# Kernel tuning notes

Hardware: AMD Instinct MI355X
Metric: run time of the kernel (lower is better)

## Reference

```python
import jax, jax.numpy as jnp
import numpy as np

S, B, E, H, O, WL, PL, T = 128, 64, 1024, 1024, 135, 64, 32, 100


def setup_inputs() -> dict:
    key = jax.random.key(0)
    ks = jax.random.split(key, 12)
    rn = lambda k, shape, s=1.0: jax.random.normal(k, shape, jnp.float32) * s
    return dict(
        encoder_states=rn(ks[0], (S, B, E)),
        encoder_hidden=rn(ks[1], (2, B, E // 2)),
        previous_poses=rn(ks[2], (PL, B, O)),
        words=rn(ks[3], (WL, B, 200)),
        real_poses_len=T,
        W_ed=rn(ks[4], (H, E), 0.02), b_ed=jnp.zeros((H,), jnp.float32),
        W_att=rn(ks[5], (H, E), 0.02), b_att=jnp.zeros((H,), jnp.float32),
        W_watt=rn(ks[6], (H, 200), 0.02), b_watt=jnp.zeros((H,), jnp.float32),
        W_ih=rn(ks[7], (3 * H, O), 0.02), W_hh=rn(ks[8], (3 * H, H), 0.02),
        b_ih=jnp.zeros((3 * H,), jnp.float32), b_hh=jnp.zeros((3 * H,), jnp.float32),
        W_out=rn(ks[9], (O, 3 * H), 0.02), b_out=jnp.zeros((O,), jnp.float32),
    )


def _gru_step(x, h, W_ih, W_hh, b_ih, b_hh):
    # PyTorch GRU cell: gates ordered (r, z, n)
    gi = x @ W_ih.T + b_ih  # [B, 3H]
    gh = h @ W_hh.T + b_hh  # [B, 3H]
    Hd = h.shape[-1]
    ir, iz, inn = gi[:, :Hd], gi[:, Hd:2 * Hd], gi[:, 2 * Hd:]
    hr, hz, hn = gh[:, :Hd], gh[:, Hd:2 * Hd], gh[:, 2 * Hd:]
    r = jax.nn.sigmoid(ir + hr)
    z = jax.nn.sigmoid(iz + hz)
    n = jnp.tanh(inn + r * hn)
    return (1.0 - z) * n + z * h


def _attend(proj, h):
    # proj: [S, B, H] (already enc_to_dec-projected), h: [B, H]
    scores = jnp.einsum('sbh,bh->bs', proj, h)
    w = jax.nn.softmax(scores, axis=1)
    return jnp.einsum('sbh,bs->bh', proj, w)  # [B, H]


def reference(encoder_states, encoder_hidden, previous_poses, words, real_poses_len,
              W_ed, b_ed, W_att, b_att, W_watt, b_watt,
              W_ih, W_hh, b_ih, b_hh, W_out, b_out):
    s, b, e = encoder_states.shape
    # take last bidirectional layer, merge directions -> [B, E]
    eh = encoder_hidden.reshape(-1, 2, b, e // 2)[-1]          # [2, B, E/2]
    h = jnp.transpose(eh, (1, 0, 2)).reshape(b, e) @ W_ed.T + b_ed  # [B, H]

    # warm-up GRU pass over previous poses (only final hidden is used)
    def warm(hc, x):
        return _gru_step(x, hc, W_ih, W_hh, b_ih, b_hh), None
    h, _ = jax.lax.scan(warm, h, previous_poses)

    # attention projections are step-invariant: hoist out of the loop
    enc_proj = encoder_states @ W_att.T + b_att   # [S, B, H]
    word_proj = words @ W_watt.T + b_watt         # [WL, B, H]

    start = previous_poses[-1]                    # [B, O]

    def step(carry, _):
        pose, hc = carry
        hc = _gru_step(pose, hc, W_ih, W_hh, b_ih, b_hh)
        ctx = _attend(enc_proj, hc)
        wctx = _attend(word_proj, hc)
        cat = jnp.concatenate([hc, ctx, wctx], axis=1)  # [B, 3H]; dropout = identity (eval)
        pose = cat @ W_out.T + b_out                    # [B, O]
        return (pose, hc), pose

    _, poses = jax.lax.scan(step, (start, h), None, length=real_poses_len)
    return poses  # [T, B, O]
```

## Files before the change

### kernel.cpp

```cpp
#include <hip/hip_runtime.h>
#include <cstdint>
#include <cstddef>

typedef unsigned short ushort_t;
typedef __attribute__((ext_vector_type(8))) short short8;
typedef __attribute__((ext_vector_type(4))) float floatx4;

#define SS 128
#define BB 64
#define EE 1024
#define HH 1024
#define OO 135
#define WLW 64
#define PLP 32
#define TT 100
#define KP 160
#define NWG 64
#define NTH 1024

#define WHH_PITCH 1032
#define WIH_PITCH 168
#define LDS_WHH   0
#define LDS_WIH   99072
#define LDS_CX    115200
#define LDS_SC    127488
#define LDS_WTS   128256
#define LDS_RED   115200
#define RED_GATE  304
#define RED_BT    1216
#define RED_REG   4864

#define FB_DTYPE 0
#define FB_FLAGS 32

static __device__ __forceinline__ float bf2f(ushort_t u) {
    union { unsigned int i; float f; } v; v.i = ((unsigned int)u) << 16; return v.f;
}
static __device__ __forceinline__ ushort_t f2bf(float f) {
    union { float f; unsigned int i; } v; v.f = f;
    unsigned int x = v.i;
    x += 0x7fffu + ((x >> 16) & 1u);
    return (ushort_t)(x >> 16);
}
static __device__ __forceinline__ float ldf(const void* p, long i, unsigned isbf) {
    if (isbf) return bf2f(((const ushort_t*)p)[i]);
    return ((const float*)p)[i];
}
static __device__ __forceinline__ short8 ldfrag(const ushort_t* p) {
    return *reinterpret_cast<const short8*>(p);
}
static __device__ __forceinline__ short8 ldfrag_l(const short* p) {
    return *reinterpret_cast<const short8*>(p);
}
static __device__ __forceinline__ int cxp(int m) {
    return ((m & 15) << 6) | (m >> 4);
}
static __device__ __forceinline__ unsigned long long sysld_u64(const void* p) {
    return __hip_atomic_load((const unsigned long long*)p, __ATOMIC_RELAXED, __HIP_MEMORY_SCOPE_AGENT);
}
static __device__ __forceinline__ void sysst_u16(ushort_t* p, ushort_t v) {
    __hip_atomic_store(p, v, __ATOMIC_RELAXED, __HIP_MEMORY_SCOPE_AGENT);
}
static __device__ __forceinline__ void sysst_u32(unsigned* p, unsigned v) {
    __hip_atomic_store(p, v, __ATOMIC_RELAXED, __HIP_MEMORY_SCOPE_SYSTEM);
}
static __device__ __forceinline__ unsigned sysld_u32(const unsigned* p) {
    return __hip_atomic_load(p, __ATOMIC_RELAXED, __HIP_MEMORY_SCOPE_SYSTEM);
}
static __device__ __forceinline__ short8 sysld_frag16(const ushort_t* p) {
    union { unsigned long long u[2]; short8 s; } r;
    r.u[0] = sysld_u64(p);
    r.u[1] = sysld_u64(p + 4);
    return r.s;
}
static __device__ __forceinline__ short8 frag_ld(const void* p, unsigned isbf,
                                                 long rowoff, int kbase, int kcap) {
    if (kbase >= kcap) {
        short8 z = {0, 0, 0, 0, 0, 0, 0, 0};
        return z;
    }
    if (isbf) return ldfrag((const ushort_t*)p + rowoff + kbase);
    const float* f = (const float*)p + rowoff + kbase;
    short8 a;
    #pragma unroll
    for (int i = 0; i < 8; ++i) a[i] = (short)f2bf(f[i]);
    return a;
}
static __device__ __forceinline__ floatx4 mfma(short8 a, short8 b, floatx4 c) {
    return __builtin_amdgcn_mfma_f32_16x16x32_bf16(a, b, c, 0, 0, 0);
}
static __device__ __forceinline__ float sigmoidf(float x) {
    x = fminf(fmaxf(x, -30.f), 30.f);
    return 1.f / (1.f + __expf(-x));
}
static __device__ __forceinline__ float tanh_f(float x) {
    x = fminf(fmaxf(x, -15.f), 15.f);
    float e = __expf(2.f * x);
    return (e - 1.f) / (e + 1.f);
}

static __device__ __forceinline__ void gbar(unsigned* flags, unsigned phase) {
    __syncthreads();
    if (threadIdx.x < 64) {
        __builtin_amdgcn_fence(__ATOMIC_RELEASE, "workgroup");
        if (threadIdx.x == 0)
            sysst_u32(&flags[(size_t)blockIdx.x * 32], phase);
        for (;;) {
            unsigned v = sysld_u32(&flags[(size_t)threadIdx.x * 32]);
            if (__all((int)(v >= phase))) break;
            __builtin_amdgcn_s_sleep(1);
        }
        __builtin_amdgcn_fence(__ATOMIC_ACQUIRE, "workgroup");
    }
    __syncthreads();
}

__global__ void k_detect(const unsigned* __restrict__ enc, unsigned* __restrict__ flag)
{
    __shared__ int cnt;
    if (threadIdx.x == 0) cnt = 0;
    __syncthreads();
    unsigned w = enc[threadIdx.x];
    unsigned ef = (w >> 7) & 0xFFu;
    if (ef >= 0x70u && ef <= 0x81u) atomicAdd(&cnt, 1);
    for (int i = threadIdx.x; i < NWG * 32; i += 256)
        sysst_u32(&flag[FB_FLAGS + i], 0u);
    __syncthreads();
    if (threadIdx.x == 0)
        flag[FB_DTYPE] = (cnt >= 200) ? 1u : 0u;
}

__global__ void k_prep(const void* __restrict__ eh, const void* __restrict__ Wih,
                       const void* __restrict__ Wout, const void* __restrict__ pp,
                       const void* __restrict__ Whh,
                       ushort_t* __restrict__ ehcat, ushort_t* __restrict__ wih_p,
                       ushort_t* __restrict__ wout_p, ushort_t* __restrict__ pp_pad,
                       ushort_t* __restrict__ pose_pad, ushort_t* __restrict__ whh_bf,
                       const unsigned* __restrict__ flag)
{
    unsigned isbf = flag[FB_DTYPE];
    long idx = (long)blockIdx.x * 256 + threadIdx.x;
    const long n1 = BB * EE;
    const long n2 = (long)3 * HH * KP;
    const long n3f = (long)144 * 3 * HH;
    const long n4 = (long)PLP * BB * KP;
    const long n5 = (long)BB * KP;
    const long n6 = (long)3 * HH * HH;
    if (idx < n1) {
        int b = (int)(idx >> 10), r = (int)(idx & 1023);
        int c = r >> 9, jj = r & 511;
        ehcat[idx] = f2bf(ldf(eh, (long)(c * BB + b) * 512 + jj, isbf));
        return;
    }
    idx -= n1;
    if (idx < n2) {
        long row = idx / KP, k = idx % KP;
        wih_p[idx] = (k < OO) ? f2bf(ldf(Wih, row * OO + k, isbf)) : (ushort_t)0; return;
    }
    idx -= n2;
    if (idx < n3f) {
        long row = idx / (3 * HH), k = idx % (3 * HH);
        wout_p[idx] = (row < OO) ? f2bf(ldf(Wout, row * (3 * HH) + k, isbf)) : (ushort_t)0; return;
    }
    idx -= n3f;
    if (idx < n4) {
        long t = idx / (BB * KP); long rem = idx % (BB * KP);
        long b = rem / KP, k = rem % KP;
        pp_pad[idx] = (k < OO) ? f2bf(ldf(pp, (t * BB + b) * OO + k, isbf)) : (ushort_t)0; return;
    }
    idx -= n4;
    if (idx < n5) { pose_pad[idx] = 0; return; }
    idx -= n5;
    if (idx < n6) { whh_bf[idx] = f2bf(ldf(Whh, idx, isbf)); return; }
}

__global__ void __launch_bounds__(256) k_gemm(
    const void* __restrict__ A, int a_bf16, int lda, int kcapA,
    const void* __restrict__ B, int b_bf16, int ldb, int kcapB,
    const void* __restrict__ biasRaw,
    float* __restrict__ outF, ushort_t* __restrict__ outB16,
    ushort_t* __restrict__ outHi, ushort_t* __restrict__ outLo,
    int ldo, int M, int N, int K, const unsigned* __restrict__ flag)
{
    unsigned isbf = flag[FB_DTYPE];
    unsigned a_isbf = a_bf16 ? 1u : isbf;
    unsigned b_isbf = b_bf16 ? 1u : isbf;
    int lane = threadIdx.x & 63;
    int wid = (blockIdx.x << 2) + (threadIdx.x >> 6);
    int ng = N >> 6;
    int mt = wid / ng, g = wid % ng;
    if (mt * 16 >= M) return;
    int col = lane & 15, quad = lane >> 4;
    long arow = (long)(mt * 16 + col) * lda;
    long brow0 = (long)((g << 6) + col) * ldb;
    long brow1 = brow0 + (long)16 * ldb;
    long brow2 = brow0 + (long)32 * ldb;
    long brow3 = brow0 + (long)48 * ldb;
    int kb = quad * 8;
    floatx4 ac0 = {0.f, 0.f, 0.f, 0.f}, ac1 = ac0, ac2 = ac0, ac3 = ac0;
    for (int k = 0; k < K; k += 32) {
        short8 av = frag_ld(A, a_isbf, arow, kb + k, kcapA);
        ac0 = mfma(av, frag_ld(B, b_isbf, brow0, kb + k, kcapB), ac0);
        ac1 = mfma(av, frag_ld(B, b_isbf, brow1, kb + k, kcapB), ac1);
        ac2 = mfma(av, frag_ld(B, b_isbf, brow2, kb + k, kcapB), ac2);
        ac3 = mfma(av, frag_ld(B, b_isbf, brow3, kb + k, kcapB), ac3);
    }
    int m0 = mt * 16 + quad * 4;
    #pragma unroll
    for (int tIdx = 0; tIdx < 4; ++tIdx) {
        floatx4 ac = (tIdx == 0) ? ac0 : (tIdx == 1) ? ac1 : (tIdx == 2) ? ac2 : ac3;
        int n = (g << 6) + tIdx * 16 + col;
        float bv = biasRaw ? ldf(biasRaw, n, isbf) : 0.f;
        #pragma unroll
        for (int r = 0; r < 4; ++r) {
            float v = ac[r] + bv;
            size_t o = (size_t)(m0 + r) * ldo + n;
            if (outF) outF[o] = v;
            if (outB16) outB16[o] = f2bf(v);
            if (outHi) {
                ushort_t hi = f2bf(v);
                outHi[o] = hi;
                outLo[o] = f2bf(v - bf2f(hi));
            }
        }
    }
}

__global__ void __launch_bounds__(1024, 4) k_persist(
    const ushort_t* encP,
    const ushort_t* wordP,
    const ushort_t* __restrict__ whh_bf, const ushort_t* __restrict__ wih_p,
    const void* __restrict__ b_ih, const void* __restrict__ b_hh,
    const ushort_t* __restrict__ wout_p,
    const void* __restrict__ b_out,
    const ushort_t* __restrict__ pp_pad, ushort_t* __restrict__ pose_pad,
    float* hFa, float* hFb, ushort_t* hhia, ushort_t* hhib,
    ushort_t* hloa, ushort_t* hlob,
    void* __restrict__ out, unsigned* flagbar)
{
    extern __shared__ char smem[];
    short* whh_lds = (short*)(smem + LDS_WHH);
    short* wih_lds = (short*)(smem + LDS_WIH);
    float* cx  = (float*)(smem + LDS_CX);
    float* sc  = (float*)(smem + LDS_SC);
    float* wts = (float*)(smem + LDS_WTS);
    float* red = (float*)(smem + LDS_RED);

    const int tid = threadIdx.x;
    const int lane = tid & 63, wv = tid >> 6;
    const int wg = blockIdx.x;
    const int col = lane & 15, quad = lane >> 4;
    const int bt = wv & 3;
    const int ks = wv >> 2;
    unsigned isbf = flagbar[FB_DTYPE];
    unsigned* flags = flagbar + FB_FLAGS;
    unsigned bphase = 0;

    float* hFs = hFa; float* hFd = hFb;
    ushort_t* hhis = hhia; ushort_t* hhid = hhib;
    ushort_t* hlos = hloa; ushort_t* hlod = hlob;

    for (int s = tid; s < 48 * 128; s += NTH) {
        int r = s >> 7;
        int ko = (s & 127) << 3;
        int g = r >> 4, rr = r & 15;
        *(short8*)(whh_lds + r * WHH_PITCH + ko) =
            ldfrag(whh_bf + (size_t)g * HH * HH + (size_t)(wg * 16 + rr) * HH + ko);
    }
    for (int s = tid; s < 48 * 20; s += NTH) {
        int r = s / 20;
        int ko = (s % 20) << 3;
        int g = r >> 4, rr = r & 15;
        *(short8*)(wih_lds + r * WIH_PITCH + ko) =
            ldfrag(wih_p + (size_t)g * HH * KP + (size_t)(wg * 16 + rr) * KP + ko);
    }
    __syncthreads();

    const int j = wg * 16 + col;
    const float bir = ldf(b_ih, j, isbf)          + ldf(b_hh, j, isbf);
    const float biz = ldf(b_ih, HH + j, isbf)     + ldf(b_hh, HH + j, isbf);
    const float bin = ldf(b_ih, 2 * HH + j, isbf);
    const float bhn = ldf(b_hh, 2 * HH + j, isbf);

    for (int t = 0; t < PLP + TT; ++t) {
        const bool dec = (t >= PLP);
        const bool warm_src = (t <= PLP);
        const ushort_t* poseA = (t < PLP)  ? (pp_pad + (size_t)t * BB * KP)
                              : (t == PLP) ? (pp_pad + (size_t)(PLP - 1) * BB * KP)
                                           : pose_pad;
        {
            const ushort_t* ah = hhis + (size_t)(bt * 16 + col) * HH + quad * 8;
            const ushort_t* al = hlos + (size_t)(bt * 16 + col) * HH + quad * 8;
            const short* w0 = whh_lds + (size_t)(0  + col) * WHH_PITCH + quad * 8;
            const short* w1 = whh_lds + (size_t)(16 + col) * WHH_PITCH + quad * 8;
            const short* w2 = whh_lds + (size_t)(32 + col) * WHH_PITCH + quad * 8;
            floatx4 aR = {0.f, 0.f, 0.f, 0.f}, aZ = aR, aNi = aR, aNh = aR;
            const int k0 = ks * 256, k1 = k0 + 256;
            #pragma unroll 4
            for (int k = k0; k < k1; k += 32) {
                short8 f0 = ldfrag_l(w0 + k), f1 = ldfrag_l(w1 + k), f2 = ldfrag_l(w2 + k);
                short8 xh = sysld_frag16(ah + k), xl = sysld_frag16(al + k);
                aR = mfma(xh, f0, aR);   aR = mfma(xl, f0, aR);
                aZ = mfma(xh, f1, aZ);   aZ = mfma(xl, f1, aZ);
                aNh = mfma(xh, f2, aNh); aNh = mfma(xl, f2, aNh);
            }
            const ushort_t* ap = poseA + (size_t)(bt * 16 + col) * KP + quad * 8;
            const short* c0 = wih_lds + (size_t)(0  + col) * WIH_PITCH + quad * 8;
            const short* c1 = wih_lds + (size_t)(16 + col) * WIH_PITCH + quad * 8;
            const short* c2 = wih_lds + (size_t)(32 + col) * WIH_PITCH + quad * 8;
            for (int k5 = ks; k5 < 5; k5 += 4) {
                int k = k5 * 32;
                short8 xp = warm_src ? ldfrag(ap + k) : sysld_frag16(ap + k);
                aR = mfma(xp, ldfrag_l(c0 + k), aR);
                aZ = mfma(xp, ldfrag_l(c1 + k), aZ);
                aNi = mfma(xp, ldfrag_l(c2 + k), aNi);
            }
            if (ks == 1 || ks == 3) {
                float* dst = red + (ks >> 1) * RED_REG + bt * RED_BT;
                #pragma unroll
                for (int r = 0; r < 4; ++r) {
                    int idx = (quad * 4 + r) * 19 + col;
                    dst[idx] = aR[r];                  dst[RED_GATE + idx] = aZ[r];
                    dst[2 * RED_GATE + idx] = aNh[r];  dst[3 * RED_GATE + idx] = aNi[r];
                }
            }
            __syncthreads();
            if (ks == 0 || ks == 2) {
                const float* sp = red + (ks >> 1) * RED_REG + bt * RED_BT;
                #pragma unroll
                for (int r = 0; r < 4; ++r) {
                    int idx = (quad * 4 + r) * 19 + col;
                    aR[r] += sp[idx];                  aZ[r] += sp[RED_GATE + idx];
                    aNh[r] += sp[2 * RED_GATE + idx];  aNi[r] += sp[3 * RED_GATE + idx];
                }
            }
            __syncthreads();
            if (ks == 2) {
                float* dst = red + bt * RED_BT;
                #pragma unroll
                for (int r = 0; r < 4; ++r) {
                    int idx = (quad * 4 + r) * 19 + col;
                    dst[idx] = aR[r];                  dst[RED_GATE + idx] = aZ[r];
                    dst[2 * RED_GATE + idx] = aNh[r];  dst[3 * RED_GATE + idx] = aNi[r];
                }
            }
            __syncthreads();
            if (ks == 0) {
                const float* sp = red + bt * RED_BT;
                #pragma unroll
                for (int r = 0; r < 4; ++r) {
                    int idx = (quad * 4 + r) * 19 + col;
                    aR[r] += sp[idx];                  aZ[r] += sp[RED_GATE + idx];
                    aNh[r] += sp[2 * RED_GATE + idx];  aNi[r] += sp[3 * RED_GATE + idx];
                }
                #pragma unroll
                for (int r = 0; r < 4; ++r) {
                    int b = bt * 16 + quad * 4 + r;
                    float hold = hFs[(size_t)b * HH + j];
                    float rg = sigmoidf(aR[r] + bir);
                    float zg = sigmoidf(aZ[r] + biz);
                    float ng = tanh_f(aNi[r] + bin + rg * (aNh[r] + bhn));
                    float hn = (1.f - zg) * ng + zg * hold;
                    hFd[(size_t)b * HH + j] = hn;
                    ushort_t hi = f2bf(hn);
                    sysst_u16(&hhid[(size_t)b * HH + j], hi);
                    sysst_u16(&hlod[(size_t)b * HH + j], f2bf(hn - bf2f(hi)));
                }
            }
        }
        { float* tf = hFs; hFs = hFd; hFd = tf; }
        { ushort_t* tp = hhis; hhis = hhid; hhid = tp;
          tp = hlos; hlos = hlod; hlod = tp; }
        ++bphase;
        gbar(flags, bphase);
        if (!dec) continue;

        {
            const int b = wg;
            if (tid < 256) {
                union { unsigned long long u; ushort_t e[4]; } h4, l4;
                h4.u = sysld_u64(hhis + (size_t)b * HH + tid * 4);
                l4.u = sysld_u64(hlos + (size_t)b * HH + tid * 4);
                #pragma unroll
                for (int i = 0; i < 4; ++i)
                    cx[cxp(tid * 4 + i)] = bf2f(h4.e[i]) + bf2f(l4.e[i]);
            }
            __syncthreads();
            float hreg[16];
            #pragma unroll
            for (int i = 0; i < 16; ++i) hreg[i] = cx[(i << 6) | lane];
            const ushort_t* rows = encP;
            #pragma unroll 2
            for (int idx = wv; idx < 192; idx += 16) {
                const ushort_t* rp = rows + ((size_t)(idx * BB + b) << 10);
                short8 v0 = ldfrag(rp + lane * 16);
                short8 v1 = ldfrag(rp + lane * 16 + 8);
                float s = 0.f;
                #pragma unroll
                for (int i = 0; i < 8; ++i) s += bf2f((ushort_t)v0[i]) * hreg[i];
                #pragma unroll
                for (int i = 0; i < 8; ++i) s += bf2f((ushort_t)v1[i]) * hreg[8 + i];
                #pragma unroll
                for (int m = 1; m < 64; m <<= 1) s += __shfl_xor(s, m);
                if (lane == 0) sc[idx] = s;
            }
            __syncthreads();
            if (wv == 0) {
                float a = sc[lane], c = sc[lane + 64];
                float mx = fmaxf(a, c);
                #pragma unroll
                for (int m = 1; m < 64; m <<= 1) mx = fmaxf(mx, __shfl_xor(mx, m));
                float e0 = __expf(a - mx), e1 = __expf(c - mx);
                float sm = e0 + e1;
                #pragma unroll
                for (int m = 1; m < 64; m <<= 1) sm += __shfl_xor(sm, m);
                float inv = 1.f / sm;
                wts[lane] = e0 * inv; wts[lane + 64] = e1 * inv;
            } else if (wv == 1) {
                float a = sc[128 + lane];
                float mx = a;
                #pragma unroll
                for (int m = 1; m < 64; m <<= 1) mx = fmaxf(mx, __shfl_xor(mx, m));
                float e0 = __expf(a - mx);
                float sm = e0;
                #pragma unroll
                for (int m = 1; m < 64; m <<= 1) sm += __shfl_xor(sm, m);
                wts[128 + lane] = e0 / sm;
            }
            __syncthreads();
            if (tid < 256) {
                float a0 = 0.f, a1 = 0.f, a2 = 0.f, a3 = 0.f;
                const ushort_t* basep = encP + ((size_t)b << 10) + tid * 4;
                #pragma unroll 8
                for (int s = 0; s < SS; ++s) {
                    float w = wts[s];
                    union { unsigned long long u; ushort_t e[4]; } v;
                    v.u = *(const unsigned long long*)(basep + ((size_t)(s * BB) << 10));
                    a0 += w * bf2f(v.e[0]); a1 += w * bf2f(v.e[1]);
                    a2 += w * bf2f(v.e[2]); a3 += w * bf2f(v.e[3]);
                }
                cx[1024 + cxp(tid * 4 + 0)] = a0; cx[1024 + cxp(tid * 4 + 1)] = a1;
                cx[1024 + cxp(tid * 4 + 2)] = a2; cx[1024 + cxp(tid * 4 + 3)] = a3;
            } else if (tid < 512) {
                int tt = tid - 256;
                float a0 = 0.f, a1 = 0.f, a2 = 0.f, a3 = 0.f;
                const ushort_t* basep = wordP + ((size_t)b << 10) + tt * 4;
                #pragma unroll 8
                for (int s = 0; s < WLW; ++s) {
                    float w = wts[128 + s];
                    union { unsigned long long u; ushort_t e[4]; } v;
                    v.u = *(const unsigned long long*)(basep + ((size_t)(s * BB) << 10));
                    a0 += w * bf2f(v.e[0]); a1 += w * bf2f(v.e[1]);
                    a2 += w * bf2f(v.e[2]); a3 += w * bf2f(v.e[3]);
                }
                cx[2048 + cxp(tt * 4 + 0)] = a0; cx[2048 + cxp(tt * 4 + 1)] = a1;
                cx[2048 + cxp(tt * 4 + 2)] = a2; cx[2048 + cxp(tt * 4 + 3)] = a3;
            }
            __syncthreads();
            float cr[48];
            #pragma unroll
            for (int c3 = 0; c3 < 3; ++c3)
                #pragma unroll
                for (int i = 0; i < 16; ++i)
                    cr[c3 * 16 + i] = cx[c3 * 1024 + (i << 6) + lane];
            int td = t - PLP;
            for (int oo = 0; oo < 9; ++oo) {
                int o = wv * 9 + oo;
                const ushort_t* wr = wout_p + (size_t)o * (3 * HH) + lane * 16;
                float s = 0.f;
                #pragma unroll
                for (int c3 = 0; c3 < 3; ++c3) {
                    short8 w8a = ldfrag(wr + c3 * 1024);
                    short8 w8b = ldfrag(wr + c3 * 1024 + 8);
                    #pragma unroll
                    for (int i = 0; i < 8; ++i) s += bf2f((ushort_t)w8a[i]) * cr[c3 * 16 + i];
                    #pragma unroll
                    for (int i = 0; i < 8; ++i) s += bf2f((ushort_t)w8b[i]) * cr[c3 * 16 + 8 + i];
                }
                #pragma unroll
                for (int m = 1; m < 64; m <<= 1) s += __shfl_xor(s, m);
                if (lane == 0) {
                    float v = s + ((o < OO) ? ldf(b_out, o, isbf) : 0.f);
                    if (o < OO) {
                        size_t oi = ((size_t)td * BB + b) * OO + o;
                        if (isbf) ((ushort_t*)out)[oi] = f2bf(v);
                        else      ((float*)out)[oi] = v;
                    }
                    sysst_u16(&pose_pad[(size_t)b * KP + o], (o < OO) ? f2bf(v) : (ushort_t)0);
                }
            }
        }
        ++bphase;
        gbar(flags, bphase);
    }
}

extern "C" void kernel_launch(void* const* d_in, const int* in_sizes, int n_in,
                              void* d_out, int out_size, void* d_ws, size_t ws_size,
                              hipStream_t stream)
{
    (void)in_sizes; (void)n_in; (void)out_size; (void)ws_size;
    const void* enc_states = d_in[0];
    const void* enc_hidden = d_in[1];
    const void* prev_poses = d_in[2];
    const void* words      = d_in[3];
    const void* W_ed  = d_in[5];
    const void* b_ed  = d_in[6];
    const void* W_att = d_in[7];
    const void* b_att = d_in[8];
    const void* W_watt = d_in[9];
    const void* b_watt = d_in[10];
    const void* W_ih  = d_in[11];
    const void* W_hh  = d_in[12];
    const void* b_ih  = d_in[13];
    const void* b_hh  = d_in[14];
    const void* W_out = d_in[15];
    const void* b_out = d_in[16];

    char* base = (char*)d_ws;
    size_t off = 0;
    auto alloc = [&](size_t bytes) -> char* {
        char* p = base + off;
        off = (off + bytes + 255) & ~(size_t)255;
        return p;
    };
    unsigned* flagbar  = (unsigned*)alloc(128 + (size_t)NWG * 128);
    ushort_t* ehcat    = (ushort_t*)alloc((size_t)BB * EE * 2);
    ushort_t* wih_p    = (ushort_t*)alloc((size_t)3 * HH * KP * 2);
    ushort_t* wout_p   = (ushort_t*)alloc((size_t)144 * 3 * HH * 2);
    ushort_t* pp_pad   = (ushort_t*)alloc((size_t)PLP * BB * KP * 2);
    ushort_t* pose_pad = (ushort_t*)alloc((size_t)BB * KP * 2);
    ushort_t* whh_bf   = (ushort_t*)alloc((size_t)3 * HH * HH * 2);
    float*    hF0      = (float*)alloc((size_t)BB * HH * 4);
    float*    hF1      = (float*)alloc((size_t)BB * HH * 4);
    ushort_t* hhi0     = (ushort_t*)alloc((size_t)BB * HH * 2);
    ushort_t* hhi1     = (ushort_t*)alloc((size_t)BB * HH * 2);
    ushort_t* hlo0     = (ushort_t*)alloc((size_t)BB * HH * 2);
    ushort_t* hlo1     = (ushort_t*)alloc((size_t)BB * HH * 2);
    ushort_t* encP     = (ushort_t*)alloc((size_t)SS * BB * HH * 2);
    ushort_t* wordP    = (ushort_t*)alloc((size_t)WLW * BB * HH * 2);

    k_detect<<<1, 256, 0, stream>>>((const unsigned*)enc_states, flagbar);

    k_prep<<<17512, 256, 0, stream>>>(enc_hidden, W_ih, W_out, prev_poses, W_hh,
                                      ehcat, wih_p, wout_p, pp_pad, pose_pad, whh_bf,
                                      flagbar);

    k_gemm<<<16, 256, 0, stream>>>(ehcat, 1, EE, EE, W_ed, 0, EE, EE, b_ed,
                                   hF0, nullptr, hhi0, hlo0, HH, BB, HH, EE, flagbar);
    k_gemm<<<2048, 256, 0, stream>>>(enc_states, 0, EE, EE, W_att, 0, EE, EE, b_att,
                                     nullptr, encP, nullptr, nullptr, HH, SS * BB, HH, EE, flagbar);
    k_gemm<<<1024, 256, 0, stream>>>(words, 0, 200, 200, W_watt, 0, 200, 200, b_watt,
                                     nullptr, wordP, nullptr, nullptr, HH, WLW * BB, HH, 224, flagbar);

    (void)hipFuncSetAttribute((const void*)k_persist,
                              hipFuncAttributeMaxDynamicSharedMemorySize, 154112);
    k_persist<<<NWG, NTH, 154112, stream>>>(encP, wordP, whh_bf, wih_p,
                                            b_ih, b_hh, wout_p, b_out, pp_pad, pose_pad,
                                            hF0, hF1, hhi0, hhi1, hlo0, hlo1,
                                            d_out, flagbar);
}
```

Measured before the change: 6.118 ms.

## Use MFMA with hi/lo bf16 split for attention scores and output projection

```diff
diff --git a/kernel.cpp b/kernel.cpp
--- a/kernel.cpp
+++ b/kernel.cpp
@@ -22,9 +22,13 @@
 #define WIH_PITCH 168
 #define LDS_WHH   0
 #define LDS_WIH   99072
-#define LDS_CX    115200
-#define LDS_SC    127488
-#define LDS_WTS   128256
+#define LDS_SC    115200
+#define LDS_WTS   115968
+#define LDS_HBH   116736
+#define LDS_HBL   118784
+#define LDS_CXH   120832
+#define LDS_CXL   124928
+#define LDS_PP    129024
 #define LDS_RED   115200
 #define RED_GATE  304
 #define RED_BT    1216
@@ -51,9 +55,6 @@
 }
 static __device__ __forceinline__ short8 ldfrag_l(const short* p) {
     return *reinterpret_cast<const short8*>(p);
-}
-static __device__ __forceinline__ int cxp(int m) {
-    return ((m & 15) << 6) | (m >> 4);
 }
 static __device__ __forceinline__ unsigned long long sysld_u64(const void* p) {
     return __hip_atomic_load((const unsigned long long*)p, __ATOMIC_RELAXED, __HIP_MEMORY_SCOPE_AGENT);
@@ -241,9 +242,13 @@
     extern __shared__ char smem[];
     short* whh_lds = (short*)(smem + LDS_WHH);
     short* wih_lds = (short*)(smem + LDS_WIH);
-    float* cx  = (float*)(smem + LDS_CX);
     float* sc  = (float*)(smem + LDS_SC);
     float* wts = (float*)(smem + LDS_WTS);
+    ushort_t* hb_hi = (ushort_t*)(smem + LDS_HBH);
+    ushort_t* hb_lo = (ushort_t*)(smem + LDS_HBL);
+    ushort_t* cx_hi = (ushort_t*)(smem + LDS_CXH);
+    ushort_t* cx_lo = (ushort_t*)(smem + LDS_CXL);
+    float* pose_part = (float*)(smem + LDS_PP);
     float* red = (float*)(smem + LDS_RED);
 
     const int tid = threadIdx.x;
@@ -378,31 +383,29 @@
         {
             const int b = wg;
             if (tid < 256) {
-                union { unsigned long long u; ushort_t e[4]; } h4, l4;
-                h4.u = sysld_u64(hhis + (size_t)b * HH + tid * 4);
-                l4.u = sysld_u64(hlos + (size_t)b * HH + tid * 4);
-                #pragma unroll
-                for (int i = 0; i < 4; ++i)
-                    cx[cxp(tid * 4 + i)] = bf2f(h4.e[i]) + bf2f(l4.e[i]);
-            }
-            __syncthreads();
-            float hreg[16];
-            #pragma unroll
-            for (int i = 0; i < 16; ++i) hreg[i] = cx[(i << 6) | lane];
+                int k0b = tid * 4;
+                unsigned long long h4 = sysld_u64(hhis + (size_t)b * HH + k0b);
+                unsigned long long l4 = sysld_u64(hlos + (size_t)b * HH + k0b);
+                *(unsigned long long*)(hb_hi + k0b) = h4;
+                *(unsigned long long*)(hb_lo + k0b) = l4;
+            }
+            __syncthreads();
             const ushort_t* rows = encP;
-            #pragma unroll 2
-            for (int idx = wv; idx < 192; idx += 16) {
-                const ushort_t* rp = rows + ((size_t)(idx * BB + b) << 10);
-                short8 v0 = ldfrag(rp + lane * 16);
-                short8 v1 = ldfrag(rp + lane * 16 + 8);
-                float s = 0.f;
-                #pragma unroll
-                for (int i = 0; i < 8; ++i) s += bf2f((ushort_t)v0[i]) * hreg[i];
-                #pragma unroll
-                for (int i = 0; i < 8; ++i) s += bf2f((ushort_t)v1[i]) * hreg[8 + i];
-                #pragma unroll
-                for (int m = 1; m < 64; m <<= 1) s += __shfl_xor(s, m);
-                if (lane == 0) sc[idx] = s;
+            if (wv < 12) {
+                const ushort_t* ap0 = rows + (((size_t)(wv * 16 + col) * BB + b) << 10) + quad * 8;
+                floatx4 acc = {0.f, 0.f, 0.f, 0.f};
+                #pragma unroll 4
+                for (int ks2 = 0; ks2 < 32; ++ks2) {
+                    short8 av = ldfrag(ap0 + ks2 * 32);
+                    short8 bh = *(const short8*)(hb_hi + ks2 * 32 + quad * 8);
+                    short8 bl = *(const short8*)(hb_lo + ks2 * 32 + quad * 8);
+                    acc = mfma(av, bh, acc);
+                    acc = mfma(av, bl, acc);
+                }
+                if (col == 0) {
+                    #pragma unroll
+                    for (int r = 0; r < 4; ++r) sc[wv * 16 + quad * 4 + r] = acc[r];
+                }
             }
             __syncthreads();
             if (wv == 0) {
@@ -439,8 +442,15 @@
                     a0 += w * bf2f(v.e[0]); a1 += w * bf2f(v.e[1]);
                     a2 += w * bf2f(v.e[2]); a3 += w * bf2f(v.e[3]);
                 }
-                cx[1024 + cxp(tid * 4 + 0)] = a0; cx[1024 + cxp(tid * 4 + 1)] = a1;
-                cx[1024 + cxp(tid * 4 + 2)] = a2; cx[1024 + cxp(tid * 4 + 3)] = a3;
+                union { unsigned long long u; ushort_t e[4]; } hi4, lo4;
+                float vv[4] = {a0, a1, a2, a3};
+                #pragma unroll
+                for (int i = 0; i < 4; ++i) {
+                    hi4.e[i] = f2bf(vv[i]);
+                    lo4.e[i] = f2bf(vv[i] - bf2f(hi4.e[i]));
+                }
+                *(unsigned long long*)(cx_hi + tid * 4) = hi4.u;
+                *(unsigned long long*)(cx_lo + tid * 4) = lo4.u;
             } else if (tid < 512) {
                 int tt = tid - 256;
                 float a0 = 0.f, a1 = 0.f, a2 = 0.f, a3 = 0.f;
@@ -453,41 +463,55 @@
                     a0 += w * bf2f(v.e[0]); a1 += w * bf2f(v.e[1]);
                     a2 += w * bf2f(v.e[2]); a3 += w * bf2f(v.e[3]);
                 }
-                cx[2048 + cxp(tt * 4 + 0)] = a0; cx[2048 + cxp(tt * 4 + 1)] = a1;
-                cx[2048 + cxp(tt * 4 + 2)] = a2; cx[2048 + cxp(tt * 4 + 3)] = a3;
-            }
-            __syncthreads();
-            float cr[48];
-            #pragma unroll
-            for (int c3 = 0; c3 < 3; ++c3)
-                #pragma unroll
-                for (int i = 0; i < 16; ++i)
-                    cr[c3 * 16 + i] = cx[c3 * 1024 + (i << 6) + lane];
+                union { unsigned long long u; ushort_t e[4]; } hi4, lo4;
+                float vv[4] = {a0, a1, a2, a3};
+                #pragma unroll
+                for (int i = 0; i < 4; ++i) {
+                    hi4.e[i] = f2bf(vv[i]);
+                    lo4.e[i] = f2bf(vv[i] - bf2f(hi4.e[i]));
+                }
+                *(unsigned long long*)(cx_hi + 1024 + tt * 4) = hi4.u;
+                *(unsigned long long*)(cx_lo + 1024 + tt * 4) = lo4.u;
+            }
+            __syncthreads();
+            #pragma unroll 2
+            for (int pass = 0; pass < 2; ++pass) {
+                if (pass == 1 && wv >= 2) break;
+                int J = (pass == 0) ? wv : 16 + wv;
+                int tile = J >> 1, kh = J & 1;
+                const ushort_t* wr = wout_p + (size_t)(tile * 16 + col) * 3072
+                                   + kh * 1536 + quad * 8;
+                floatx4 acc = {0.f, 0.f, 0.f, 0.f};
+                #pragma unroll 4
+                for (int ks2 = 0; ks2 < 48; ++ks2) {
+                    int kk = kh * 1536 + ks2 * 32;
+                    short8 av = ldfrag(wr + ks2 * 32);
+                    const ushort_t* bh;
+                    const ushort_t* bl;
+                    if (kk < 1024) { bh = hb_hi + kk + quad * 8; bl = hb_lo + kk + quad * 8; }
+                    else           { bh = cx_hi + (kk - 1024) + quad * 8;
+                                     bl = cx_lo + (kk - 1024) + quad * 8; }
+                    acc = mfma(av, *(const short8*)bh, acc);
+                    acc = mfma(av, *(const short8*)bl, acc);
+                }
+                if (col == 0) {
+                    #pragma unroll
+                    for (int r = 0; r < 4; ++r)
+                        pose_part[J * 16 + quad * 4 + r] = acc[r];
+                }
+            }
+            __syncthreads();
             int td = t - PLP;
-            for (int oo = 0; oo < 9; ++oo) {
-                int o = wv * 9 + oo;
-                const ushort_t* wr = wout_p + (size_t)o * (3 * HH) + lane * 16;
-                float s = 0.f;
-                #pragma unroll
-                for (int c3 = 0; c3 < 3; ++c3) {
-                    short8 w8a = ldfrag(wr + c3 * 1024);
-                    short8 w8b = ldfrag(wr + c3 * 1024 + 8);
-                    #pragma unroll
-                    for (int i = 0; i < 8; ++i) s += bf2f((ushort_t)w8a[i]) * cr[c3 * 16 + i];
-                    #pragma unroll
-                    for (int i = 0; i < 8; ++i) s += bf2f((ushort_t)w8b[i]) * cr[c3 * 16 + 8 + i];
-                }
-                #pragma unroll
-                for (int m = 1; m < 64; m <<= 1) s += __shfl_xor(s, m);
-                if (lane == 0) {
-                    float v = s + ((o < OO) ? ldf(b_out, o, isbf) : 0.f);
-                    if (o < OO) {
-                        size_t oi = ((size_t)td * BB + b) * OO + o;
-                        if (isbf) ((ushort_t*)out)[oi] = f2bf(v);
-                        else      ((float*)out)[oi] = v;
-                    }
-                    sysst_u16(&pose_pad[(size_t)b * KP + o], (o < OO) ? f2bf(v) : (ushort_t)0);
-                }
+            if (tid < 144) {
+                int o = tid, T = o >> 4, r = o & 15;
+                float v = pose_part[(T * 2) * 16 + r] + pose_part[(T * 2 + 1) * 16 + r]
+                        + ((o < OO) ? ldf(b_out, o, isbf) : 0.f);
+                if (o < OO) {
+                    size_t oi = ((size_t)td * BB + b) * OO + o;
+                    if (isbf) ((ushort_t*)out)[oi] = f2bf(v);
+                    else      ((float*)out)[oi] = v;
+                }
+                sysst_u16(&pose_pad[(size_t)b * KP + o], (o < OO) ? f2bf(v) : (ushort_t)0);
             }
         }
         ++bphase;
```

New measurement: 7.917 ms. 1.29x slower.

## Repartition GRU step: stream weights from global, stage h tile in LDS

Applied to the files above, without the earlier changes.

```diff
diff --git a/kernel.cpp b/kernel.cpp
--- a/kernel.cpp
+++ b/kernel.cpp
@@ -18,17 +18,16 @@
 #define NWG 64
 #define NTH 1024
 
-#define WHH_PITCH 1032
-#define WIH_PITCH 168
-#define LDS_WHH   0
-#define LDS_WIH   99072
-#define LDS_CX    115200
-#define LDS_SC    127488
-#define LDS_WTS   128256
-#define LDS_RED   115200
+#define LDS_HSH   0
+#define LDS_HSL   33024
+#define LDS_CX    66048
+#define LDS_SC    78336
+#define LDS_WTS   79104
+#define LDS_RED   66048
 #define RED_GATE  304
-#define RED_BT    1216
+#define RED_JS    1216
 #define RED_REG   4864
+#define SMEM_SZ   104960
 
 #define FB_DTYPE 0
 #define FB_FLAGS 32
@@ -239,8 +238,8 @@
     void* __restrict__ out, unsigned* flagbar)
 {
     extern __shared__ char smem[];
-    short* whh_lds = (short*)(smem + LDS_WHH);
-    short* wih_lds = (short*)(smem + LDS_WIH);
+    short* hsh = (short*)(smem + LDS_HSH);
+    short* hsl = (short*)(smem + LDS_HSL);
     float* cx  = (float*)(smem + LDS_CX);
     float* sc  = (float*)(smem + LDS_SC);
     float* wts = (float*)(smem + LDS_WTS);
@@ -250,8 +249,10 @@
     const int lane = tid & 63, wv = tid >> 6;
     const int wg = blockIdx.x;
     const int col = lane & 15, quad = lane >> 4;
-    const int bt = wv & 3;
-    const int ks = wv >> 2;
+    const int jt  = (wg & 7) | ((wg >> 5) << 3);
+    const int bt2 = (wg >> 3) & 3;
+    const int js  = wv & 3;
+    const int ks4 = wv >> 2;
     unsigned isbf = flagbar[FB_DTYPE];
     unsigned* flags = flagbar + FB_FLAGS;
     unsigned bphase = 0;
@@ -260,27 +261,20 @@
     ushort_t* hhis = hhia; ushort_t* hhid = hhib;
     ushort_t* hlos = hloa; ushort_t* hlod = hlob;
 
-    for (int s = tid; s < 48 * 128; s += NTH) {
-        int r = s >> 7;
-        int ko = (s & 127) << 3;
-        int g = r >> 4, rr = r & 15;
-        *(short8*)(whh_lds + r * WHH_PITCH + ko) =
-            ldfrag(whh_bf + (size_t)g * HH * HH + (size_t)(wg * 16 + rr) * HH + ko);
-    }
-    for (int s = tid; s < 48 * 20; s += NTH) {
-        int r = s / 20;
-        int ko = (s % 20) << 3;
-        int g = r >> 4, rr = r & 15;
-        *(short8*)(wih_lds + r * WIH_PITCH + ko) =
-            ldfrag(wih_p + (size_t)g * HH * KP + (size_t)(wg * 16 + rr) * KP + ko);
-    }
-    __syncthreads();
-
-    const int j = wg * 16 + col;
-    const float bir = ldf(b_ih, j, isbf)          + ldf(b_hh, j, isbf);
-    const float biz = ldf(b_ih, HH + j, isbf)     + ldf(b_hh, HH + j, isbf);
-    const float bin = ldf(b_ih, 2 * HH + j, isbf);
-    const float bhn = ldf(b_hh, 2 * HH + j, isbf);
+    const int jme = jt * 64 + js * 16 + col;
+    const float bir = ldf(b_ih, jme, isbf)          + ldf(b_hh, jme, isbf);
+    const float biz = ldf(b_ih, HH + jme, isbf)     + ldf(b_hh, HH + jme, isbf);
+    const float bin = ldf(b_ih, 2 * HH + jme, isbf);
+    const float bhn = ldf(b_hh, 2 * HH + jme, isbf);
+
+    const ushort_t* w0g = whh_bf + (size_t)jme * HH + quad * 8;
+    const ushort_t* w1g = whh_bf + (size_t)HH * HH + (size_t)jme * HH + quad * 8;
+    const ushort_t* w2g = whh_bf + 2 * (size_t)HH * HH + (size_t)jme * HH + quad * 8;
+    const ushort_t* c0g = wih_p + (size_t)jme * KP + quad * 8;
+    const ushort_t* c1g = wih_p + ((size_t)HH + jme) * KP + quad * 8;
+    const ushort_t* c2g = wih_p + ((size_t)2 * HH + jme) * KP + quad * 8;
+    const short* ahh = hsh + col * 1032 + quad * 8;
+    const short* ahl = hsl + col * 1032 + quad * 8;
 
     for (int t = 0; t < PLP + TT; ++t) {
         const bool dec = (t >= PLP);
@@ -289,34 +283,39 @@
                               : (t == PLP) ? (pp_pad + (size_t)(PLP - 1) * BB * KP)
                                            : pose_pad;
         {
-            const ushort_t* ah = hhis + (size_t)(bt * 16 + col) * HH + quad * 8;
-            const ushort_t* al = hlos + (size_t)(bt * 16 + col) * HH + quad * 8;
-            const short* w0 = whh_lds + (size_t)(0  + col) * WHH_PITCH + quad * 8;
-            const short* w1 = whh_lds + (size_t)(16 + col) * WHH_PITCH + quad * 8;
-            const short* w2 = whh_lds + (size_t)(32 + col) * WHH_PITCH + quad * 8;
+            #pragma unroll
+            for (int r4 = 0; r4 < 4; ++r4) {
+                int idx = r4 * NTH + tid;
+                int arr = idx >> 11;
+                int rem = idx & 2047;
+                int brow = rem >> 7;
+                int ch  = rem & 127;
+                const ushort_t* srcb = arr ? hlos : hhis;
+                short8 v = sysld_frag16(srcb + (size_t)(bt2 * 16 + brow) * HH + ch * 8);
+                short* dstb = arr ? hsl : hsh;
+                *(short8*)(dstb + brow * 1032 + ch * 8) = v;
+            }
+            __syncthreads();
             floatx4 aR = {0.f, 0.f, 0.f, 0.f}, aZ = aR, aNi = aR, aNh = aR;
-            const int k0 = ks * 256, k1 = k0 + 256;
+            const int k0 = ks4 * 256, k1 = k0 + 256;
             #pragma unroll 4
             for (int k = k0; k < k1; k += 32) {
-                short8 f0 = ldfrag_l(w0 + k), f1 = ldfrag_l(w1 + k), f2 = ldfrag_l(w2 + k);
-                short8 xh = sysld_frag16(ah + k), xl = sysld_frag16(al + k);
+                short8 f0 = ldfrag(w0g + k), f1 = ldfrag(w1g + k), f2 = ldfrag(w2g + k);
+                short8 xh = ldfrag_l(ahh + k), xl = ldfrag_l(ahl + k);
                 aR = mfma(xh, f0, aR);   aR = mfma(xl, f0, aR);
                 aZ = mfma(xh, f1, aZ);   aZ = mfma(xl, f1, aZ);
                 aNh = mfma(xh, f2, aNh); aNh = mfma(xl, f2, aNh);
             }
-            const ushort_t* ap = poseA + (size_t)(bt * 16 + col) * KP + quad * 8;
-            const short* c0 = wih_lds + (size_t)(0  + col) * WIH_PITCH + quad * 8;
-            const short* c1 = wih_lds + (size_t)(16 + col) * WIH_PITCH + quad * 8;
-            const short* c2 = wih_lds + (size_t)(32 + col) * WIH_PITCH + quad * 8;
-            for (int k5 = ks; k5 < 5; k5 += 4) {
+            const ushort_t* ap = poseA + (size_t)(bt2 * 16 + col) * KP + quad * 8;
+            for (int k5 = ks4; k5 < 5; k5 += 4) {
                 int k = k5 * 32;
                 short8 xp = warm_src ? ldfrag(ap + k) : sysld_frag16(ap + k);
-                aR = mfma(xp, ldfrag_l(c0 + k), aR);
-                aZ = mfma(xp, ldfrag_l(c1 + k), aZ);
-                aNi = mfma(xp, ldfrag_l(c2 + k), aNi);
-            }
-            if (ks == 1 || ks == 3) {
-                float* dst = red + (ks >> 1) * RED_REG + bt * RED_BT;
+                aR = mfma(xp, ldfrag(c0g + k), aR);
+                aZ = mfma(xp, ldfrag(c1g + k), aZ);
+                aNi = mfma(xp, ldfrag(c2g + k), aNi);
+            }
+            if (ks4 == 1 || ks4 == 3) {
+                float* dst = red + (ks4 >> 1) * RED_REG + js * RED_JS;
                 #pragma unroll
                 for (int r = 0; r < 4; ++r) {
                     int idx = (quad * 4 + r) * 19 + col;
@@ -325,8 +324,8 @@
                 }
             }
             __syncthreads();
-            if (ks == 0 || ks == 2) {
-                const float* sp = red + (ks >> 1) * RED_REG + bt * RED_BT;
+            if (ks4 == 0 || ks4 == 2) {
+                const float* sp = red + (ks4 >> 1) * RED_REG + js * RED_JS;
                 #pragma unroll
                 for (int r = 0; r < 4; ++r) {
                     int idx = (quad * 4 + r) * 19 + col;
@@ -335,8 +334,8 @@
                 }
             }
             __syncthreads();
-            if (ks == 2) {
-                float* dst = red + bt * RED_BT;
+            if (ks4 == 2) {
+                float* dst = red + js * RED_JS;
                 #pragma unroll
                 for (int r = 0; r < 4; ++r) {
                     int idx = (quad * 4 + r) * 19 + col;
@@ -345,8 +344,8 @@
                 }
             }
             __syncthreads();
-            if (ks == 0) {
-                const float* sp = red + bt * RED_BT;
+            if (ks4 == 0) {
+                const float* sp = red + js * RED_JS;
                 #pragma unroll
                 for (int r = 0; r < 4; ++r) {
                     int idx = (quad * 4 + r) * 19 + col;
@@ -355,16 +354,16 @@
                 }
                 #pragma unroll
                 for (int r = 0; r < 4; ++r) {
-                    int b = bt * 16 + quad * 4 + r;
-                    float hold = hFs[(size_t)b * HH + j];
+                    int b = bt2 * 16 + quad * 4 + r;
+                    float hold = hFs[(size_t)b * HH + jme];
                     float rg = sigmoidf(aR[r] + bir);
                     float zg = sigmoidf(aZ[r] + biz);
                     float ng = tanh_f(aNi[r] + bin + rg * (aNh[r] + bhn));
                     float hn = (1.f - zg) * ng + zg * hold;
-                    hFd[(size_t)b * HH + j] = hn;
+                    hFd[(size_t)b * HH + jme] = hn;
                     ushort_t hi = f2bf(hn);
-                    sysst_u16(&hhid[(size_t)b * HH + j], hi);
-                    sysst_u16(&hlod[(size_t)b * HH + j], f2bf(hn - bf2f(hi)));
+                    sysst_u16(&hhid[(size_t)b * HH + jme], hi);
+                    sysst_u16(&hlod[(size_t)b * HH + jme], f2bf(hn - bf2f(hi)));
                 }
             }
         }
@@ -554,9 +553,9 @@
                                      nullptr, wordP, nullptr, nullptr, HH, WLW * BB, HH, 224, flagbar);
 
     (void)hipFuncSetAttribute((const void*)k_persist,
-                              hipFuncAttributeMaxDynamicSharedMemorySize, 154112);
-    k_persist<<<NWG, NTH, 154112, stream>>>(encP, wordP, whh_bf, wih_p,
-                                            b_ih, b_hh, wout_p, b_out, pp_pad, pose_pad,
-                                            hF0, hF1, hhi0, hhi1, hlo0, hlo1,
-                                            d_out, flagbar);
-}
+                              hipFuncAttributeMaxDynamicSharedMemorySize, SMEM_SZ);
+    k_persist<<<NWG, NTH, SMEM_SZ, stream>>>(encP, wordP, whh_bf, wih_p,
+                                             b_ih, b_hh, wout_p, b_out, pp_pad, pose_pad,
+                                             hF0, hF1, hhi0, hhi1, hlo0, hlo1,
+                                             d_out, flagbar);
+}
```

Result: slower. 8.828 ms (+44.3%).
